# Optimization experiments

Hardware: AMD Instinct MI355X
Metric: run time of the kernel (lower is better)

Reference implementation:

```python
import jax, jax.numpy as jnp
import numpy as np

N_NODES = 100000
N_EDGES = 1000000
IN_FEATS = 64
HID = 128
NUM_CLASSES = 10


def setup_inputs() -> dict:
    key = jax.random.key(0)
    ks = jax.random.split(key, 8)
    x = jax.random.normal(ks[0], (N_NODES, IN_FEATS), dtype=jnp.float32)
    edge_index = jax.random.randint(ks[1], (2, N_EDGES), 0, N_NODES, dtype=jnp.int64)
    # Glorot-style init scale for weights
    def w(k, fan_in, fan_out):
        s = (2.0 / (fan_in + fan_out)) ** 0.5
        return jax.random.normal(k, (fan_in, fan_out), dtype=jnp.float32) * s
    return {
        "x": x,
        "edge_index": edge_index,
        "W1": w(ks[2], IN_FEATS, HID),
        "b1": jnp.zeros((HID,), dtype=jnp.float32),
        "W2": w(ks[3], HID, HID),
        "b2": jnp.zeros((HID,), dtype=jnp.float32),
        "Wl": w(ks[4], HID, NUM_CLASSES),
        "bl": jnp.zeros((NUM_CLASSES,), dtype=jnp.float32),
    }


def _gcn_conv(x, src, dst, norm, W, b, num_nodes):
    # PyG GCNConv: h = x W, then out_i = sum_{j->i} norm_ij * h_j + b
    h = x @ W  # [N, out]
    msgs = h[src] * norm[:, None]  # gather + scale  [E+N, out]
    out = jax.ops.segment_sum(msgs, dst, num_segments=num_nodes)
    return out + b


def reference(x, edge_index, W1, b1, W2, b2, Wl, bl):
    N = x.shape[0]
    loops = jnp.arange(N, dtype=edge_index.dtype)
    src = jnp.concatenate([edge_index[0], loops])  # source nodes (messages from)
    dst = jnp.concatenate([edge_index[1], loops])  # target nodes (aggregate at)
    # symmetric normalization: deg over targets (includes self-loops)
    deg = jax.ops.segment_sum(jnp.ones(dst.shape, dtype=x.dtype), dst, num_segments=N)
    dinv = jnp.where(deg > 0, jax.lax.rsqrt(deg), 0.0)
    norm = dinv[src] * dinv[dst]  # [E+N]

    h = jax.nn.relu(_gcn_conv(x, src, dst, norm, W1, b1, N))
    h = jax.nn.relu(_gcn_conv(h, src, dst, norm, W2, b2, N))
    return jax.nn.log_softmax(h @ Wl + bl, axis=1)
```

## Files before the change

kernel.cpp:

```cpp
#include <hip/hip_runtime.h>
#include <hip/hip_fp16.h>
#include <math.h>

#define NUM_CLASSES 10

#define BSH 9
#define BSZ 512
#define BCAP 6144

typedef _Float16 half8  __attribute__((ext_vector_type(8)));
typedef _Float16 half4t __attribute__((ext_vector_type(4)));
typedef float    floatx4 __attribute__((ext_vector_type(4)));

__global__ __launch_bounds__(256) void prep_kernel(const float* __restrict__ W1,
                                                   const float* __restrict__ W2,
                                                   const float* __restrict__ Wlc,
                                                   _Float16* __restrict__ W1t,
                                                   _Float16* __restrict__ W2t,
                                                   _Float16* __restrict__ Wct,
                                                   int* __restrict__ fill, int nbuck) {
    const int b = blockIdx.x, tid = threadIdx.x;
    if (b == 0 && tid < nbuck) fill[tid] = 0;
    if (b < 32) {
        int i = b * 256 + tid;
        int k = i >> 7, c = i & 127;
        W1t[c * 72 + k] = (_Float16)W1[i];
    } else if (b < 96) {
        int i = (b - 32) * 256 + tid;
        int k = i >> 7, c = i & 127;
        W2t[c * 136 + k] = (_Float16)W2[i];
    } else {
        for (int i = tid; i < 16 * 136; i += 256) {
            int c = i / 136, k = i - c * 136;
            float v = (c < NUM_CLASSES && k < 128) ? Wlc[k * NUM_CLASSES + c] : 0.0f;
            Wct[i] = (_Float16)v;
        }
    }
}

__global__ __launch_bounds__(256) void csr_p1_kernel(const int* __restrict__ src,
                                                     const int* __restrict__ dst,
                                                     int* __restrict__ bucket_fill,
                                                     unsigned* __restrict__ pairs, int E) {
    __shared__ int hist[256], base[256], cur[256];
    const int tid = threadIdx.x;
    hist[tid] = 0;
    cur[tid] = 0;
    __syncthreads();
    const int bb = blockIdx.x * 2048;
    unsigned pk[8];
    int bk[8];
    int cnt = 0;
#pragma unroll
    for (int i = 0; i < 8; ++i) {
        int idx = bb + i * 256 + tid;
        if (idx < E) {
            int s = src[idx], d = dst[idx];
            bk[i] = d >> BSH;
            pk[i] = ((unsigned)s << BSH) | (unsigned)(d & (BSZ - 1));
            atomicAdd(&hist[bk[i]], 1);
            cnt = i + 1;
        }
    }
    __syncthreads();
    if (hist[tid] > 0) base[tid] = atomicAdd(&bucket_fill[tid], hist[tid]);
    __syncthreads();
#pragma unroll
    for (int i = 0; i < 8; ++i) {
        if (i < cnt) {
            int b = bk[i];
            int r = atomicAdd(&cur[b], 1) + base[b];
            if (r < BCAP) pairs[(size_t)b * BCAP + r] = pk[i];
        }
    }
}

__global__ __launch_bounds__(256) void csr_p2_kernel(const int* __restrict__ bucket_fill,
                                                     const unsigned* __restrict__ pairs,
                                                     const float* __restrict__ x,
                                                     int* __restrict__ rowstart,
                                                     float* __restrict__ dinv,
                                                     int* __restrict__ csr_src,
                                                     __half2* __restrict__ xs_h,
                                                     int N, int nbuck) {
    __shared__ int cnt[BSZ], excl[BSZ], cur[BSZ];
    __shared__ int s1[256];
    const int tid = threadIdx.x;
    const int b = blockIdx.x;
    const int node0 = b << BSH;
    const int nodes_b = min(BSZ, N - node0);

    cnt[tid] = 0; cnt[tid + 256] = 0;
    cur[tid] = 0; cur[tid + 256] = 0;
    s1[tid] = (tid < b) ? bucket_fill[tid] : 0;
    __syncthreads();
    for (int off = 128; off > 0; off >>= 1) {
        if (tid < off) s1[tid] += s1[tid + off];
        __syncthreads();
    }
    const int bbase = s1[0];
    const int ne = bucket_fill[b];
    __syncthreads();

    const unsigned* bp = pairs + (size_t)b * BCAP;
    for (int i = tid; i < ne; i += 256)
        atomicAdd(&cnt[bp[i] & (BSZ - 1)], 1);
    __syncthreads();
    int c0 = cnt[2 * tid], c1 = cnt[2 * tid + 1];
    s1[tid] = c0 + c1;
    __syncthreads();
    for (int off = 1; off < 256; off <<= 1) {
        int t = (tid >= off) ? s1[tid - off] : 0;
        __syncthreads();
        s1[tid] += t;
        __syncthreads();
    }
    int ex = s1[tid] - (c0 + c1);
    excl[2 * tid] = ex;
    excl[2 * tid + 1] = ex + c0;
    __syncthreads();
    for (int i = tid; i < nodes_b; i += 256) {
        rowstart[node0 + i] = bbase + excl[i];
        dinv[node0 + i] = rsqrtf((float)cnt[i] + 1.0f);
    }
    if (b == nbuck - 1 && tid == 0) rowstart[N] = bbase + ne;
    for (int i = tid; i < nodes_b * 32; i += 256) {
        int ln = i >> 5;
        float d = rsqrtf((float)cnt[ln] + 1.0f);
        float2 v = ((const float2*)x)[(size_t)node0 * 32 + i];
        xs_h[(size_t)node0 * 32 + i] = __floats2half2_rn(v.x * d, v.y * d);
    }
    for (int i = tid; i < ne; i += 256) {
        unsigned p = bp[i];
        int d = (int)(p & (BSZ - 1));
        int r = atomicAdd(&cur[d], 1);
        csr_src[bbase + excl[d] + r] = (int)(p >> BSH);
    }
}

template <int F>
__global__ __launch_bounds__(256) void gather_h_kernel(const __half2* __restrict__ hs,
                                                       const float* __restrict__ dinv,
                                                       const int* __restrict__ rowstart,
                                                       const int* __restrict__ csr_src,
                                                       __half2* __restrict__ out, int N) {
    constexpr int F2 = F / 2;
    int node = (blockIdx.x * 256 + threadIdx.x) >> 6;
    int lane = threadIdx.x & 63;
    if (node >= N) return;
    int f2 = lane & (F2 - 1);

    int beg = rowstart[node];
    int end = rowstart[node + 1];
    int deg = end - beg;

    float2 self = __half22float2(hs[(size_t)node * F2 + f2]);
    int lim = deg < 64 ? deg : 64;
    int myidx = (lane < lim) ? csr_src[beg + lane] : node;
    int itersUp = (lim + 7) & ~7;
    float comp = (float)(1 - (itersUp - lim));
    float2 acc;
    acc.x = self.x * comp;
    acc.y = self.y * comp;

    for (int j = 0; j < itersUp; j += 8) {
        int s[8];
#pragma unroll
        for (int u = 0; u < 8; ++u) s[u] = __shfl(myidx, j + u);
        float2 v[8];
#pragma unroll
        for (int u = 0; u < 8; ++u) v[u] = __half22float2(hs[(size_t)s[u] * F2 + f2]);
#pragma unroll
        for (int u = 0; u < 8; ++u) { acc.x += v[u].x; acc.y += v[u].y; }
    }
    for (int j = beg + 64; j < end; ++j) {
        int s = csr_src[j];
        float2 v = __half22float2(hs[(size_t)s * F2 + f2]);
        acc.x += v.x;
        acc.y += v.y;
    }
    if (F == 128 || lane < 32) {
        float d = dinv[node];
        out[(size_t)node * F2 + f2] = __floats2half2_rn(d * acc.x, d * acc.y);
    }
}

template <int K, bool SCALE_OUT>
__global__ __launch_bounds__(256) void gemm_mfma_kernel(const _Float16* __restrict__ In,
                                                        const _Float16* __restrict__ Wt,
                                                        const float* __restrict__ bias,
                                                        const float* __restrict__ dinv,
                                                        _Float16* __restrict__ Out, int N) {
    constexpr int KP = K + 8;
    constexpr int NC = K / 32;
    __shared__ _Float16 Wl[128 * KP];
    __shared__ float bias_s[128];
    const int tid = threadIdx.x;

    for (int i = tid; i < (128 * KP) / 8; i += 256)
        ((floatx4*)Wl)[i] = ((const floatx4*)Wt)[i];
    if (tid < 128) bias_s[tid] = bias[tid];
    __syncthreads();

    const int lane = tid & 63;
    const int wave = tid >> 6;
    const int q = lane >> 4;
    const int l15 = lane & 15;

#pragma unroll
    for (int iter = 0; iter < 2; ++iter) {
        int myrow = blockIdx.x * 128 + iter * 64 + wave * 16 + l15;
        int r = myrow < N ? myrow : N - 1;
        half8 xf[NC];
#pragma unroll
        for (int c = 0; c < NC; ++c)
            xf[c] = *(const half8*)(In + (size_t)r * K + c * 32 + q * 8);
        floatx4 acc[8];
#pragma unroll
        for (int t = 0; t < 8; ++t) acc[t] = (floatx4){0.f, 0.f, 0.f, 0.f};
#pragma unroll
        for (int c = 0; c < NC; ++c) {
#pragma unroll
            for (int t = 0; t < 8; ++t) {
                half8 wf = *(const half8*)(Wl + (t * 16 + l15) * KP + c * 32 + q * 8);
                acc[t] = __builtin_amdgcn_mfma_f32_16x16x32_f16(wf, xf[c], acc[t], 0, 0, 0);
            }
        }
        if (myrow < N) {
            float sc = SCALE_OUT ? dinv[myrow] : 1.0f;
#pragma unroll
            for (int t = 0; t < 8; ++t) {
                int c0 = t * 16 + q * 4;
                floatx4 bv = *(const floatx4*)&bias_s[c0];
                half4t h;
#pragma unroll
                for (int j = 0; j < 4; ++j)
                    h[j] = (_Float16)(sc * fmaxf(acc[t][j] + bv[j], 0.0f));
                *(half4t*)(Out + (size_t)myrow * 128 + c0) = h;
            }
        }
    }
}

__global__ __launch_bounds__(256) void gemm_final_kernel(const _Float16* __restrict__ In,
                                                         const _Float16* __restrict__ Wt,
                                                         const float* __restrict__ bias,
                                                         const _Float16* __restrict__ Wct,
                                                         const float* __restrict__ bl,
                                                         float* __restrict__ out, int N) {
    constexpr int K = 128, KP = 136, NC = 4;
    __shared__ _Float16 Wl[128 * KP];
    __shared__ _Float16 Wc[16 * KP];
    __shared__ float bias_s[128];
    __shared__ float bl_s[16];
    __shared__ _Float16 act_s[4][16 * KP];
    const int tid = threadIdx.x;

    for (int i = tid; i < (128 * KP) / 8; i += 256)
        ((floatx4*)Wl)[i] = ((const floatx4*)Wt)[i];
    for (int i = tid; i < (16 * KP) / 8; i += 256)
        ((floatx4*)Wc)[i] = ((const floatx4*)Wct)[i];
    if (tid < 128) bias_s[tid] = bias[tid];
    if (tid < 16) bl_s[tid] = (tid < NUM_CLASSES) ? bl[tid] : -1e30f;
    __syncthreads();

    const int lane = tid & 63;
    const int wave = tid >> 6;
    const int q = lane >> 4;
    const int l15 = lane & 15;
    _Float16* As = act_s[wave];

    half8 wcf[NC];
#pragma unroll
    for (int c = 0; c < NC; ++c)
        wcf[c] = *(const half8*)(Wc + l15 * KP + c * 32 + q * 8);
    float myclsb[4];
#pragma unroll
    for (int reg = 0; reg < 4; ++reg) myclsb[reg] = bl_s[q * 4 + reg];

#pragma unroll
    for (int iter = 0; iter < 2; ++iter) {
        int rowbase = blockIdx.x * 128 + iter * 64 + wave * 16;
        int myrow = rowbase + l15;
        int r = myrow < N ? myrow : N - 1;
        half8 xf[NC];
#pragma unroll
        for (int c = 0; c < NC; ++c)
            xf[c] = *(const half8*)(In + (size_t)r * K + c * 32 + q * 8);
        floatx4 acc[8];
#pragma unroll
        for (int t = 0; t < 8; ++t) acc[t] = (floatx4){0.f, 0.f, 0.f, 0.f};
#pragma unroll
        for (int c = 0; c < NC; ++c) {
#pragma unroll
            for (int t = 0; t < 8; ++t) {
                half8 wf = *(const half8*)(Wl + (t * 16 + l15) * KP + c * 32 + q * 8);
                acc[t] = __builtin_amdgcn_mfma_f32_16x16x32_f16(wf, xf[c], acc[t], 0, 0, 0);
            }
        }
#pragma unroll
        for (int t = 0; t < 8; ++t) {
            int c0 = t * 16 + q * 4;
            floatx4 bv = *(const floatx4*)&bias_s[c0];
            half4t h;
#pragma unroll
            for (int j = 0; j < 4; ++j)
                h[j] = (_Float16)fmaxf(acc[t][j] + bv[j], 0.0f);
            *(half4t*)&As[l15 * KP + c0] = h;
        }
        floatx4 lg = (floatx4){0.f, 0.f, 0.f, 0.f};
#pragma unroll
        for (int c = 0; c < NC; ++c) {
            half8 af = *(const half8*)(As + l15 * KP + c * 32 + q * 8);
            lg = __builtin_amdgcn_mfma_f32_16x16x32_f16(wcf[c], af, lg, 0, 0, 0);
        }
        if (myrow < N) {
            float v[4];
#pragma unroll
            for (int reg = 0; reg < 4; ++reg) v[reg] = lg[reg] + myclsb[reg];
            float mx = fmaxf(fmaxf(v[0], v[1]), fmaxf(v[2], v[3]));
            mx = fmaxf(mx, __shfl_xor(mx, 16));
            mx = fmaxf(mx, __shfl_xor(mx, 32));
            float sm = expf(v[0] - mx) + expf(v[1] - mx) + expf(v[2] - mx) + expf(v[3] - mx);
            sm += __shfl_xor(sm, 16);
            sm += __shfl_xor(sm, 32);
            float lse = mx + logf(sm);
#pragma unroll
            for (int reg = 0; reg < 4; ++reg) {
                int cls = q * 4 + reg;
                if (cls < NUM_CLASSES)
                    out[(size_t)myrow * NUM_CLASSES + cls] = v[reg] - lse;
            }
        }
    }
}

extern "C" void kernel_launch(void* const* d_in, const int* in_sizes, int n_in,
                              void* d_out, int out_size, void* d_ws, size_t ws_size,
                              hipStream_t stream) {
    const float* x  = (const float*)d_in[0];
    const int*   ei = (const int*)d_in[1];
    const float* W1 = (const float*)d_in[2];
    const float* b1 = (const float*)d_in[3];
    const float* W2 = (const float*)d_in[4];
    const float* b2 = (const float*)d_in[5];
    const float* Wlc = (const float*)d_in[6];
    const float* bl = (const float*)d_in[7];
    float* out = (float*)d_out;

    const int N = in_sizes[0] / 64;
    const int E = in_sizes[1] / 2;
    const int* src = ei;
    const int* dst = ei + E;
    const int nbuck = (N + BSZ - 1) >> BSH;

    char* ws = (char*)d_ws;
    int*      bucket_fill = (int*)(ws + 0);
    int*      rowstart    = (int*)(ws + 4096);
    float*    dinv        = (float*)(ws + 524288);
    _Float16* W1t         = (_Float16*)(ws + 1048576);
    _Float16* W2t         = (_Float16*)(ws + 1069056);
    _Float16* Wct         = (_Float16*)(ws + 1103872);
    unsigned* pairs       = (unsigned*)(ws + 2097152);
    int*      csr_src     = (int*)(ws + 12582912);
    char*     region1     = ws + 16777216;
    char*     region2     = ws + 68157440;
    __half2*  xs_h = (__half2*)region1;
    __half2*  g1h  = (__half2*)(region1 + 13631488);
    __half2*  g2h  = (__half2*)region1;
    __half2*  a1_h = (__half2*)region2;

    const int P1B = (E + 2047) / 2048;
    const int GB  = (N + 127) / 128;
    const int WVB = (N + 3) / 4;

    prep_kernel<<<97, 256, 0, stream>>>(W1, W2, Wlc, W1t, W2t, Wct, bucket_fill, nbuck);
    csr_p1_kernel<<<P1B, 256, 0, stream>>>(src, dst, bucket_fill, pairs, E);
    csr_p2_kernel<<<nbuck, 256, 0, stream>>>(bucket_fill, pairs, x, rowstart, dinv,
                                             csr_src, xs_h, N, nbuck);

    gather_h_kernel<64><<<WVB, 256, 0, stream>>>(xs_h, dinv, rowstart, csr_src, g1h, N);
    gemm_mfma_kernel<64, true><<<GB, 256, 0, stream>>>((const _Float16*)g1h, W1t, b1, dinv,
                                                       (_Float16*)a1_h, N);

    gather_h_kernel<128><<<WVB, 256, 0, stream>>>(a1_h, dinv, rowstart, csr_src, g2h, N);
    gemm_final_kernel<<<GB, 256, 0, stream>>>((const _Float16*)g2h, W2t, b2, Wct, bl, out, N);
}
```

Measured before the change: 250.9 us.

## Shrink CSR buckets to 128 nodes and precompute bucket bases in a scan kernel

Bucket size in the two-pass CSR build drops from 512 to 128 nodes, so the pass-2 kernel launches about 782 blocks instead of 196 and fills the GPU better. The per-block prefix-sum reduction over all earlier bucket counts is replaced by a separate single-block scan kernel that writes the bucket base offsets. In exchange, pass 1 keeps a 1024-entry shared histogram with more global atomics per block, and there is one extra kernel launch. Only 128 of the 256 threads in each pass-2 block take part in the per-node scan.

Measured after the change: 228.6 us. 8.9% less time.

```diff
diff --git a/kernel.cpp b/kernel.cpp
--- a/kernel.cpp
+++ b/kernel.cpp
@@ -4,9 +4,10 @@
 
 #define NUM_CLASSES 10
 
-#define BSH 9
-#define BSZ 512
-#define BCAP 6144
+#define BSH 7
+#define BSZ 128
+#define BCAP 1792
+#define NBMAX 1024
 
 typedef _Float16 half8  __attribute__((ext_vector_type(8)));
 typedef _Float16 half4t __attribute__((ext_vector_type(4)));
@@ -20,7 +21,9 @@
                                                    _Float16* __restrict__ Wct,
                                                    int* __restrict__ fill, int nbuck) {
     const int b = blockIdx.x, tid = threadIdx.x;
-    if (b == 0 && tid < nbuck) fill[tid] = 0;
+    if (b == 0) {
+        for (int i = tid; i < nbuck; i += 256) fill[i] = 0;
+    }
     if (b < 32) {
         int i = b * 256 + tid;
         int k = i >> 7, c = i & 127;
@@ -42,10 +45,9 @@
                                                      const int* __restrict__ dst,
                                                      int* __restrict__ bucket_fill,
                                                      unsigned* __restrict__ pairs, int E) {
-    __shared__ int hist[256], base[256], cur[256];
+    __shared__ int hist[NBMAX], base[NBMAX], cur[NBMAX];
     const int tid = threadIdx.x;
-    hist[tid] = 0;
-    cur[tid] = 0;
+    for (int i = tid; i < NBMAX; i += 256) { hist[i] = 0; cur[i] = 0; }
     __syncthreads();
     const int bb = blockIdx.x * 2048;
     unsigned pk[8];
@@ -63,7 +65,8 @@
         }
     }
     __syncthreads();
-    if (hist[tid] > 0) base[tid] = atomicAdd(&bucket_fill[tid], hist[tid]);
+    for (int i = tid; i < NBMAX; i += 256)
+        if (hist[i] > 0) base[i] = atomicAdd(&bucket_fill[i], hist[i]);
     __syncthreads();
 #pragma unroll
     for (int i = 0; i < 8; ++i) {
@@ -75,7 +78,33 @@
     }
 }
 
+__global__ __launch_bounds__(256) void scan_base_kernel(const int* __restrict__ fill,
+                                                        int* __restrict__ bbase, int nbuck) {
+    __shared__ int s1[256];
+    const int tid = threadIdx.x;
+    const int i0 = tid * 4;
+    int v[4];
+#pragma unroll
+    for (int j = 0; j < 4; ++j) v[j] = (i0 + j < nbuck) ? fill[i0 + j] : 0;
+    int t = v[0] + v[1] + v[2] + v[3];
+    s1[tid] = t;
+    __syncthreads();
+    for (int off = 1; off < 256; off <<= 1) {
+        int u = (tid >= off) ? s1[tid - off] : 0;
+        __syncthreads();
+        s1[tid] += u;
+        __syncthreads();
+    }
+    int run = s1[tid] - t;
+#pragma unroll
+    for (int j = 0; j < 4; ++j) {
+        if (i0 + j < nbuck) { bbase[i0 + j] = run; run += v[j]; }
+    }
+    if (tid == 255) bbase[nbuck] = s1[255];
+}
+
 __global__ __launch_bounds__(256) void csr_p2_kernel(const int* __restrict__ bucket_fill,
+                                                     const int* __restrict__ bucket_base,
                                                      const unsigned* __restrict__ pairs,
                                                      const float* __restrict__ x,
                                                      int* __restrict__ rowstart,
@@ -84,46 +113,39 @@
                                                      __half2* __restrict__ xs_h,
                                                      int N, int nbuck) {
     __shared__ int cnt[BSZ], excl[BSZ], cur[BSZ];
-    __shared__ int s1[256];
+    __shared__ int s1[BSZ];
     const int tid = threadIdx.x;
     const int b = blockIdx.x;
     const int node0 = b << BSH;
     const int nodes_b = min(BSZ, N - node0);
 
-    cnt[tid] = 0; cnt[tid + 256] = 0;
-    cur[tid] = 0; cur[tid + 256] = 0;
-    s1[tid] = (tid < b) ? bucket_fill[tid] : 0;
-    __syncthreads();
-    for (int off = 128; off > 0; off >>= 1) {
-        if (tid < off) s1[tid] += s1[tid + off];
-        __syncthreads();
-    }
-    const int bbase = s1[0];
+    if (tid < BSZ) { cnt[tid] = 0; cur[tid] = 0; }
+    __syncthreads();
+    const int bbase = bucket_base[b];
     const int ne = bucket_fill[b];
-    __syncthreads();
 
     const unsigned* bp = pairs + (size_t)b * BCAP;
     for (int i = tid; i < ne; i += 256)
         atomicAdd(&cnt[bp[i] & (BSZ - 1)], 1);
     __syncthreads();
-    int c0 = cnt[2 * tid], c1 = cnt[2 * tid + 1];
-    s1[tid] = c0 + c1;
-    __syncthreads();
-    for (int off = 1; off < 256; off <<= 1) {
-        int t = (tid >= off) ? s1[tid - off] : 0;
+    int c = (tid < BSZ) ? cnt[tid] : 0;
+    if (tid < BSZ) s1[tid] = c;
+    __syncthreads();
+    for (int off = 1; off < BSZ; off <<= 1) {
+        int t = (tid < BSZ && tid >= off) ? s1[tid - off] : 0;
         __syncthreads();
-        s1[tid] += t;
+        if (tid < BSZ) s1[tid] += t;
         __syncthreads();
     }
-    int ex = s1[tid] - (c0 + c1);
-    excl[2 * tid] = ex;
-    excl[2 * tid + 1] = ex + c0;
-    __syncthreads();
-    for (int i = tid; i < nodes_b; i += 256) {
-        rowstart[node0 + i] = bbase + excl[i];
-        dinv[node0 + i] = rsqrtf((float)cnt[i] + 1.0f);
+    if (tid < BSZ) excl[tid] = s1[tid] - c;
+    __syncthreads();
+
+    if (tid < nodes_b) {
+        rowstart[node0 + tid] = bbase + excl[tid];
+        dinv[node0 + tid] = rsqrtf((float)cnt[tid] + 1.0f);
     }
     if (b == nbuck - 1 && tid == 0) rowstart[N] = bbase + ne;
+
     for (int i = tid; i < nodes_b * 32; i += 256) {
         int ln = i >> 5;
         float d = rsqrtf((float)cnt[ln] + 1.0f);
@@ -361,6 +383,7 @@
     _Float16* W1t         = (_Float16*)(ws + 1048576);
     _Float16* W2t         = (_Float16*)(ws + 1069056);
     _Float16* Wct         = (_Float16*)(ws + 1103872);
+    int*      bucket_base = (int*)(ws + 1110016);
     unsigned* pairs       = (unsigned*)(ws + 2097152);
     int*      csr_src     = (int*)(ws + 12582912);
     char*     region1     = ws + 16777216;
@@ -376,8 +399,9 @@
 
     prep_kernel<<<97, 256, 0, stream>>>(W1, W2, Wlc, W1t, W2t, Wct, bucket_fill, nbuck);
     csr_p1_kernel<<<P1B, 256, 0, stream>>>(src, dst, bucket_fill, pairs, E);
-    csr_p2_kernel<<<nbuck, 256, 0, stream>>>(bucket_fill, pairs, x, rowstart, dinv,
-                                             csr_src, xs_h, N, nbuck);
+    scan_base_kernel<<<1, 256, 0, stream>>>(bucket_fill, bucket_base, nbuck);
+    csr_p2_kernel<<<nbuck, 256, 0, stream>>>(bucket_fill, bucket_base, pairs, x, rowstart,
+                                             dinv, csr_src, xs_h, N, nbuck);
 
     gather_h_kernel<64><<<WVB, 256, 0, stream>>>(xs_h, dinv, rowstart, csr_src, g1h, N);
     gemm_mfma_kernel<64, true><<<GB, 256, 0, stream>>>((const _Float16*)g1h, W1t, b1, dinv,
```
